# Kernel optimization log

Measured on AMD Instinct MI355X. Metric: run time of the kernel, lower is better.

## Reference

```python
import jax, jax.numpy as jnp
import numpy as np

V, E, U, D = 32000, 128, 256, 256
B, T = 128, 1024


def setup_inputs() -> dict:
    key = jax.random.key(0)
    k_tok, k_emb, k_wk, k_wr, k_wd = jax.random.split(key, 5)
    tokens = jax.random.randint(k_tok, (B, T), 0, V, dtype=jnp.int32)
    emb_table = jax.random.normal(k_emb, (V, E), dtype=jnp.float32) * 0.02
    Wk = jax.random.normal(k_wk, (E, 4 * U), dtype=jnp.float32) * (1.0 / np.sqrt(E))
    Wr = jax.random.normal(k_wr, (U, 4 * U), dtype=jnp.float32) * (1.0 / np.sqrt(U))
    # Keras unit_forget_bias: forget-gate bias initialized to ones (gate order i,f,g,o)
    b = jnp.concatenate([jnp.zeros((U,), jnp.float32), jnp.ones((U,), jnp.float32), jnp.zeros((2 * U,), jnp.float32)])
    Wd = jax.random.normal(k_wd, (U, D), dtype=jnp.float32) * (1.0 / np.sqrt(U))
    bd = jnp.zeros((D,), jnp.float32)
    return {"tokens": tokens, "emb_table": emb_table, "Wk": Wk, "Wr": Wr, "b": b, "Wd": Wd, "bd": bd}


def _masked_lstm(x, mask, Wk, Wr, b):
    # x: [B,T,E], mask: [B,T] bool. Keras semantics: masked steps pass
    # previous h as output and leave (h, c) unchanged.
    units = Wr.shape[0]
    bsz = x.shape[0]
    xT = jnp.swapaxes(x, 0, 1)          # [T,B,E]
    mT = jnp.swapaxes(mask, 0, 1)       # [T,B]

    def step(carry, inp):
        h, c = carry
        xt, mt = inp
        z = xt @ Wk + h @ Wr + b        # [B,4U]
        i, f, g, o = jnp.split(z, 4, axis=-1)
        i = jax.nn.sigmoid(i)
        f = jax.nn.sigmoid(f)
        g = jnp.tanh(g)
        o = jax.nn.sigmoid(o)
        c_new = f * c + i * g
        h_new = o * jnp.tanh(c_new)
        m = mt[:, None]
        h2 = jnp.where(m, h_new, h)
        c2 = jnp.where(m, c_new, c)
        return (h2, c2), h2

    h0 = jnp.zeros((bsz, units), x.dtype)
    c0 = jnp.zeros((bsz, units), x.dtype)
    _, outs = jax.lax.scan(step, (h0, c0), (xT, mT))
    return jnp.swapaxes(outs, 0, 1)     # [B,T,U]


def reference(tokens, emb_table, Wk, Wr, b, Wd, bd):
    # Embedding (mask_zero=True); dropout layers are identity at inference.
    x = emb_table[tokens]               # [B,T,E]
    mask = tokens != 0                  # [B,T]
    h = _masked_lstm(x, mask, Wk, Wr, b)  # [B,T,U]
    y = jax.nn.relu(h @ Wd + bd)        # TimeDistributed Dense(relu) -> [B,T,D]
    return y
```

## Files before the change

### kernel.cpp

```cpp
#include <hip/hip_runtime.h>
#include <cstddef>


typedef unsigned int u32x4 __attribute__((ext_vector_type(4)));

constexpr int TLEN = 1024;
constexpr int EDIM = 128;
constexpr int UDIM = 256;
constexpr int DDIM = 256;

constexpr int BPB  = 8;
constexpr int UPB  = 8;
constexpr int ZCOL = 32;
constexpr int HXROW = 432;
constexpr int ZROW = 36;

__device__ unsigned long long g_pktA[2][128][256];
__device__ unsigned long long g_pktB[2][128][256];

__device__ __forceinline__ int pidx(int k) { return ((k >> 5) * 36) + (k & 31); }

__device__ __forceinline__ u32x4 pkt_load_ic(const unsigned long long* p) {
  u32x4 v;
  asm volatile("global_load_dwordx4 %0, %1, off sc0 sc1" : "=v"(v) : "v"(p));
  return v;
}
__device__ __forceinline__ u32x4 pkt_load_l2(const unsigned long long* p) {
  u32x4 v;
  asm volatile("global_load_dwordx4 %0, %1, off sc0" : "=v"(v) : "v"(p));
  return v;
}
#define PKT_WAIT4(a, b, c, d) \
  asm volatile("s_waitcnt vmcnt(0)" : "+v"(a), "+v"(b), "+v"(c), "+v"(d) :: "memory")
#define TAGS_OK() \
  ((p0[1] == want) & (p0[3] == want) & (p1[1] == want) & (p1[3] == want) & \
   (p2[1] == want) & (p2[3] == want) & (p3[1] == want) & (p3[3] == want))

__device__ __forceinline__ float rowsum16(float v) {
  v += __int_as_float(
      __builtin_amdgcn_mov_dpp(__float_as_int(v), 0x121, 0xf, 0xf, true));
  v += __int_as_float(
      __builtin_amdgcn_mov_dpp(__float_as_int(v), 0x122, 0xf, 0xf, true));
  v += __int_as_float(
      __builtin_amdgcn_mov_dpp(__float_as_int(v), 0x124, 0xf, 0xf, true));
  v += __int_as_float(
      __builtin_amdgcn_mov_dpp(__float_as_int(v), 0x128, 0xf, 0xf, true));
  return v;
}

__global__ __launch_bounds__(256, 2) void we_lstm(
    const int* __restrict__ tokens, const float* __restrict__ emb,
    const float* __restrict__ Wk, const float* __restrict__ Wr,
    const float* __restrict__ bz, float* __restrict__ out)
{
  __shared__ float hx[2][BPB][HXROW];
  __shared__ float zs[BPB][ZROW];
  __shared__ float bias_s[ZCOL];

  const int tid = threadIdx.x;
  const int bid = blockIdx.x;
  const int bg  = ((bid & 7) << 1) | ((bid >> 8) & 1);
  const int ug  = (bid >> 3) & 31;
  const int b0  = bg * BPB;
  const int u0  = ug * UPB;

  const int ksl = tid & 15;
  const int cq  = (tid >> 4) & 7;
  const int bh  = tid >> 7;

  float w[96];
#pragma unroll
  for (int i = 0; i < 6; ++i)
#pragma unroll
    for (int j = 0; j < 4; ++j) {
      const int k = ksl * 4 + i * 64 + j;
#pragma unroll
      for (int cc = 0; cc < 4; ++cc) {
        const int c   = cq * 4 + cc;
        const int col = ((c >> 3) << 8) + u0 + (c & 7);
        w[(i * 4 + j) * 4 + cc] =
            (k < UDIM) ? Wr[k * 1024 + col] : Wk[(k - UDIM) * 1024 + col];
      }
    }
  if (tid < ZCOL) bias_s[tid] = bz[((tid >> 3) << 8) + u0 + (tid & 7)];

  float creg = 0.f;
  const int gb = tid >> 3, gu = tid & 7;
  const int xb = tid >> 5, xe = (tid & 31) << 2;
  const int up = tid & 127, bq = (tid >> 7) * 4;

  bool use_local = true;

  float4 xv = *(const float4*)&emb[(size_t)tokens[(b0 + xb) * TLEN] * EDIM + xe];
  int tk_g = (tid < 64) ? tokens[(b0 + gb) * TLEN] : 1;

  for (int it = 0; it < TLEN; ++it) {
    const int cur = it & 1;

    *(float4*)&hx[cur][xb][pidx(UDIM + xe)] = xv;
    __syncthreads();

    float acc[4][4];
#pragma unroll
    for (int r = 0; r < 4; ++r) {
      acc[r][0] = 0.f; acc[r][1] = 0.f; acc[r][2] = 0.f; acc[r][3] = 0.f;
    }
#pragma unroll
    for (int i = 4; i < 6; ++i) {
      const int hoff = pidx(ksl * 4 + i * 64);
      float4 hv[4];
#pragma unroll
      for (int r = 0; r < 4; ++r)
        hv[r] = *(const float4*)&hx[cur][bh * 4 + r][hoff];
#pragma unroll
      for (int j = 0; j < 4; ++j)
#pragma unroll
        for (int r = 0; r < 4; ++r) {
          const float hval = (j == 0) ? hv[r].x : (j == 1) ? hv[r].y
                             : (j == 2) ? hv[r].z : hv[r].w;
#pragma unroll
          for (int cc = 0; cc < 4; ++cc)
            acc[r][cc] += hval * w[(i * 4 + j) * 4 + cc];
        }
    }

    u32x4 p0, p1, p2, p3;
    const unsigned want = (unsigned)it;
    const int rp = (it + 1) & 1;
    if (it > 0) {
      if (use_local) {
        p0 = pkt_load_l2(&g_pktA[rp][b0 + bq + 0][2 * up]);
        p1 = pkt_load_l2(&g_pktA[rp][b0 + bq + 1][2 * up]);
        p2 = pkt_load_l2(&g_pktA[rp][b0 + bq + 2][2 * up]);
        p3 = pkt_load_l2(&g_pktA[rp][b0 + bq + 3][2 * up]);
      } else {
        p0 = pkt_load_ic(&g_pktB[rp][b0 + bq + 0][2 * up]);
        p1 = pkt_load_ic(&g_pktB[rp][b0 + bq + 1][2 * up]);
        p2 = pkt_load_ic(&g_pktB[rp][b0 + bq + 2][2 * up]);
        p3 = pkt_load_ic(&g_pktB[rp][b0 + bq + 3][2 * up]);
      }
    }

    float4 xv_n;
    int tk_g_n = 1;
    if (it + 1 < TLEN) {
      const int tk_x = tokens[(b0 + xb) * TLEN + it + 1];
      xv_n = *(const float4*)&emb[(size_t)tk_x * EDIM + xe];
      if (tid < 64) tk_g_n = tokens[(b0 + gb) * TLEN + it + 1];
    }

    const int ho = pidx(2 * up);
    if (it > 0) {
      PKT_WAIT4(p0, p1, p2, p3);
      bool ok = TAGS_OK();
      if (use_local) {
        int rounds = 0;
        while (!ok && rounds < 8) {
          __builtin_amdgcn_s_sleep(1);
          p0 = pkt_load_l2(&g_pktA[rp][b0 + bq + 0][2 * up]);
          p1 = pkt_load_l2(&g_pktA[rp][b0 + bq + 1][2 * up]);
          p2 = pkt_load_l2(&g_pktA[rp][b0 + bq + 2][2 * up]);
          p3 = pkt_load_l2(&g_pktA[rp][b0 + bq + 3][2 * up]);
          PKT_WAIT4(p0, p1, p2, p3);
          ok = TAGS_OK();
          ++rounds;
        }
        if (!ok) use_local = false;
      }
      while (!ok) {
        p0 = pkt_load_ic(&g_pktB[rp][b0 + bq + 0][2 * up]);
        p1 = pkt_load_ic(&g_pktB[rp][b0 + bq + 1][2 * up]);
        p2 = pkt_load_ic(&g_pktB[rp][b0 + bq + 2][2 * up]);
        p3 = pkt_load_ic(&g_pktB[rp][b0 + bq + 3][2 * up]);
        PKT_WAIT4(p0, p1, p2, p3);
        ok = TAGS_OK();
        if (!ok) __builtin_amdgcn_s_sleep(1);
      }
      *(float2*)&hx[cur][bq + 0][ho] =
          make_float2(__uint_as_float(p0[0]), __uint_as_float(p0[2]));
      *(float2*)&hx[cur][bq + 1][ho] =
          make_float2(__uint_as_float(p1[0]), __uint_as_float(p1[2]));
      *(float2*)&hx[cur][bq + 2][ho] =
          make_float2(__uint_as_float(p2[0]), __uint_as_float(p2[2]));
      *(float2*)&hx[cur][bq + 3][ho] =
          make_float2(__uint_as_float(p3[0]), __uint_as_float(p3[2]));
    } else {
#pragma unroll
      for (int jj = 0; jj < 4; ++jj)
        *(float2*)&hx[cur][bq + jj][ho] = make_float2(0.f, 0.f);
    }
    __syncthreads();

#pragma unroll
    for (int i = 0; i < 4; ++i) {
      const int hoff = pidx(ksl * 4 + i * 64);
      float4 hv[4];
#pragma unroll
      for (int r = 0; r < 4; ++r)
        hv[r] = *(const float4*)&hx[cur][bh * 4 + r][hoff];
#pragma unroll
      for (int j = 0; j < 4; ++j)
#pragma unroll
        for (int r = 0; r < 4; ++r) {
          const float hval = (j == 0) ? hv[r].x : (j == 1) ? hv[r].y
                             : (j == 2) ? hv[r].z : hv[r].w;
#pragma unroll
          for (int cc = 0; cc < 4; ++cc)
            acc[r][cc] += hval * w[(i * 4 + j) * 4 + cc];
        }
    }

#pragma unroll
    for (int r = 0; r < 4; ++r)
#pragma unroll
      for (int cc = 0; cc < 4; ++cc)
        acc[r][cc] = rowsum16(acc[r][cc]);
    if (ksl == 0) {
#pragma unroll
      for (int r = 0; r < 4; ++r)
        *(float4*)&zs[bh * 4 + r][cq * 4] =
            make_float4(acc[r][0], acc[r][1], acc[r][2], acc[r][3]);
    }
    __syncthreads();

    if (tid < 64) {
      const float zi = zs[gb][gu]      + bias_s[gu];
      const float zf = zs[gb][8 + gu]  + bias_s[8 + gu];
      const float zg = zs[gb][16 + gu] + bias_s[16 + gu];
      const float zo = zs[gb][24 + gu] + bias_s[24 + gu];
      const float gi = 1.f / (1.f + __expf(-zi));
      const float gf = 1.f / (1.f + __expf(-zf));
      const float gg = 1.f - 2.f / (1.f + __expf(2.f * zg));
      const float go = 1.f / (1.f + __expf(-zo));
      const float cn = gf * creg + gi * gg;
      const float th = 1.f - 2.f / (1.f + __expf(2.f * cn));
      const float hn = go * th;
      const bool msk = (tk_g != 0);
      const float hold = hx[cur][gb][pidx(u0 + gu)];
      const float h2 = msk ? hn : hold;
      creg = msk ? cn : creg;
      const unsigned long long pkt =
          ((unsigned long long)(unsigned)(it + 1) << 32) | __float_as_uint(h2);
      __hip_atomic_store(&g_pktA[cur][b0 + gb][u0 + gu], pkt, __ATOMIC_RELAXED,
                         __HIP_MEMORY_SCOPE_WORKGROUP);
      __hip_atomic_store(&g_pktB[cur][b0 + gb][u0 + gu], pkt, __ATOMIC_RELAXED,
                         __HIP_MEMORY_SCOPE_AGENT);
      __builtin_nontemporal_store(
          h2, &out[((size_t)(b0 + gb) * TLEN + it) * DDIM + u0 + gu]);
    }
    xv = xv_n;
    tk_g = tk_g_n;
  }
}

__global__ __launch_bounds__(256, 2) void we_proj(
    const float* __restrict__ Wd, const float* __restrict__ bd,
    float* __restrict__ out)
{
  __shared__ float hs[32][260];
  __shared__ float ws[32][260];
  __shared__ float bds[DDIM];

  const int tid = threadIdx.x;
  const size_t row0 = (size_t)blockIdx.x * 32;

#pragma unroll
  for (int j2 = 0; j2 < 8; ++j2) {
    const int idx = tid + j2 * 256;
    const int r = idx >> 6;
    const int cq = idx & 63;
    *(float4*)&hs[r][cq * 4] = *(const float4*)&out[(row0 + r) * DDIM + cq * 4];
  }
  bds[tid] = bd[tid];

  const int rg = tid >> 5;
  const int c0 = (tid & 31) * 8;
  float acc[4][8];
#pragma unroll
  for (int i = 0; i < 4; ++i)
#pragma unroll
    for (int c = 0; c < 8; ++c) acc[i][c] = 0.f;

  for (int kt = 0; kt < 8; ++kt) {
    __syncthreads();
#pragma unroll
    for (int j2 = 0; j2 < 8; ++j2) {
      const int idx = tid + j2 * 256;
      const int kk = idx >> 6;
      const int cq = idx & 63;
      *(float4*)&ws[kk][cq * 4] =
          *(const float4*)&Wd[(size_t)(kt * 32 + kk) * DDIM + cq * 4];
    }
    __syncthreads();
#pragma unroll
    for (int kk = 0; kk < 32; ++kk) {
      const float4 wv0 = *(const float4*)&ws[kk][c0];
      const float4 wv1 = *(const float4*)&ws[kk][c0 + 4];
#pragma unroll
      for (int i = 0; i < 4; ++i) {
        const float hval = hs[rg + i * 8][kt * 32 + kk];
        acc[i][0] += hval * wv0.x; acc[i][1] += hval * wv0.y;
        acc[i][2] += hval * wv0.z; acc[i][3] += hval * wv0.w;
        acc[i][4] += hval * wv1.x; acc[i][5] += hval * wv1.y;
        acc[i][6] += hval * wv1.z; acc[i][7] += hval * wv1.w;
      }
    }
  }
#pragma unroll
  for (int i = 0; i < 4; ++i) {
    float4 y0, y1;
    y0.x = fmaxf(acc[i][0] + bds[c0 + 0], 0.f);
    y0.y = fmaxf(acc[i][1] + bds[c0 + 1], 0.f);
    y0.z = fmaxf(acc[i][2] + bds[c0 + 2], 0.f);
    y0.w = fmaxf(acc[i][3] + bds[c0 + 3], 0.f);
    y1.x = fmaxf(acc[i][4] + bds[c0 + 4], 0.f);
    y1.y = fmaxf(acc[i][5] + bds[c0 + 5], 0.f);
    y1.z = fmaxf(acc[i][6] + bds[c0 + 6], 0.f);
    y1.w = fmaxf(acc[i][7] + bds[c0 + 7], 0.f);
    const size_t orow = (row0 + rg + i * 8) * DDIM;
    *(float4*)&out[orow + c0]     = y0;
    *(float4*)&out[orow + c0 + 4] = y1;
  }
}

extern "C" void kernel_launch(void* const* d_in, const int* in_sizes, int n_in,
                              void* d_out, int out_size, void* d_ws, size_t ws_size,
                              hipStream_t stream) {
  const int*   tokens = (const int*)d_in[0];
  const float* emb    = (const float*)d_in[1];
  const float* Wk     = (const float*)d_in[2];
  const float* Wr     = (const float*)d_in[3];
  const float* bz     = (const float*)d_in[4];
  const float* Wd     = (const float*)d_in[5];
  const float* bd     = (const float*)d_in[6];
  float* out = (float*)d_out;
  (void)in_sizes; (void)n_in; (void)out_size; (void)d_ws; (void)ws_size;
  hipLaunchKernelGGL(we_lstm, dim3(512), dim3(256), 0, stream,
                     tokens, emb, Wk, Wr, bz, out);
  hipLaunchKernelGGL(we_proj, dim3(128 * TLEN / 32), dim3(256), 0, stream,
                     Wd, bd, out);
}
```

Measured before the change: 3.696 ms.

## Interleave two batch groups per block to hide cross-block h exchange latency

Each workgroup now handles two 8-row batch groups (A and B) in alternation instead of one, halving the grid to 256 blocks with occupancy 1. While one group computes its recurrent matvec, the packet loads for the other group's previous hidden state are already in flight. This hides the inter-block polling latency behind useful compute. The cost is fewer resident waves and the loss of the earlier split where the input-projection part was computed before the wait. The spin-retry budget on the local L2 path is also doubled.

```diff
diff --git a/kernel.cpp b/kernel.cpp
--- a/kernel.cpp
+++ b/kernel.cpp
@@ -48,7 +48,7 @@
   return v;
 }
 
-__global__ __launch_bounds__(256, 2) void we_lstm(
+__global__ __launch_bounds__(256, 1) void we_lstm(
     const int* __restrict__ tokens, const float* __restrict__ emb,
     const float* __restrict__ Wk, const float* __restrict__ Wr,
     const float* __restrict__ bz, float* __restrict__ out)
@@ -59,9 +59,10 @@
 
   const int tid = threadIdx.x;
   const int bid = blockIdx.x;
-  const int bg  = ((bid & 7) << 1) | ((bid >> 8) & 1);
-  const int ug  = (bid >> 3) & 31;
-  const int b0  = bg * BPB;
+  const int pg  = bid & 7;
+  const int ug  = bid >> 3;
+  const int b0A = pg * 16;
+  const int b0B = pg * 16 + 8;
   const int u0  = ug * UPB;
 
   const int ksl = tid & 15;
@@ -84,20 +85,69 @@
     }
   if (tid < ZCOL) bias_s[tid] = bz[((tid >> 3) << 8) + u0 + (tid & 7)];
 
-  float creg = 0.f;
+  float cregA = 0.f, cregB = 0.f;
   const int gb = tid >> 3, gu = tid & 7;
   const int xb = tid >> 5, xe = (tid & 31) << 2;
   const int up = tid & 127, bq = (tid >> 7) * 4;
 
   bool use_local = true;
 
-  float4 xv = *(const float4*)&emb[(size_t)tokens[(b0 + xb) * TLEN] * EDIM + xe];
-  int tk_g = (tid < 64) ? tokens[(b0 + gb) * TLEN] : 1;
-
-  for (int it = 0; it < TLEN; ++it) {
-    const int cur = it & 1;
-
-    *(float4*)&hx[cur][xb][pidx(UDIM + xe)] = xv;
+  float4 xvA = *(const float4*)&emb[(size_t)tokens[(b0A + xb) * TLEN] * EDIM + xe];
+  float4 xvB = *(const float4*)&emb[(size_t)tokens[(b0B + xb) * TLEN] * EDIM + xe];
+  int tkA = (tid < 64) ? tokens[(b0A + gb) * TLEN] : 1;
+  int tkB = (tid < 64) ? tokens[(b0B + gb) * TLEN] : 1;
+
+  u32x4 pA0, pA1, pA2, pA3, pB0, pB1, pB2, pB3;
+
+  auto run_phase = [&](const int b0c, float (*hxc)[HXROW], float& creg,
+                       int& tk_g, float4& xv,
+                       u32x4& p0, u32x4& p1, u32x4& p2, u32x4& p3,
+                       const int b0n,
+                       u32x4& q0, u32x4& q1, u32x4& q2, u32x4& q3,
+                       const int it, const int itn) {
+    const int rp = (it + 1) & 1;
+    const unsigned want = (unsigned)it;
+    const int ho = pidx(2 * up);
+
+    if (it > 0) {
+      PKT_WAIT4(p0, p1, p2, p3);
+      bool ok = TAGS_OK();
+      if (!ok && use_local) {
+        int rounds = 0;
+        do {
+          __builtin_amdgcn_s_sleep(1);
+          p0 = pkt_load_l2(&g_pktA[rp][b0c + bq + 0][2 * up]);
+          p1 = pkt_load_l2(&g_pktA[rp][b0c + bq + 1][2 * up]);
+          p2 = pkt_load_l2(&g_pktA[rp][b0c + bq + 2][2 * up]);
+          p3 = pkt_load_l2(&g_pktA[rp][b0c + bq + 3][2 * up]);
+          PKT_WAIT4(p0, p1, p2, p3);
+          ok = TAGS_OK();
+        } while (!ok && ++rounds < 16);
+        if (!ok) use_local = false;
+      }
+      while (!ok) {
+        p0 = pkt_load_ic(&g_pktB[rp][b0c + bq + 0][2 * up]);
+        p1 = pkt_load_ic(&g_pktB[rp][b0c + bq + 1][2 * up]);
+        p2 = pkt_load_ic(&g_pktB[rp][b0c + bq + 2][2 * up]);
+        p3 = pkt_load_ic(&g_pktB[rp][b0c + bq + 3][2 * up]);
+        PKT_WAIT4(p0, p1, p2, p3);
+        ok = TAGS_OK();
+        if (!ok) __builtin_amdgcn_s_sleep(1);
+      }
+      *(float2*)&hxc[bq + 0][ho] =
+          make_float2(__uint_as_float(p0[0]), __uint_as_float(p0[2]));
+      *(float2*)&hxc[bq + 1][ho] =
+          make_float2(__uint_as_float(p1[0]), __uint_as_float(p1[2]));
+      *(float2*)&hxc[bq + 2][ho] =
+          make_float2(__uint_as_float(p2[0]), __uint_as_float(p2[2]));
+      *(float2*)&hxc[bq + 3][ho] =
+          make_float2(__uint_as_float(p3[0]), __uint_as_float(p3[2]));
+    } else {
+#pragma unroll
+      for (int jj = 0; jj < 4; ++jj)
+        *(float2*)&hxc[bq + jj][ho] = make_float2(0.f, 0.f);
+    }
+    *(float4*)&hxc[xb][pidx(UDIM + xe)] = xv;
     __syncthreads();
 
     float acc[4][4];
@@ -106,12 +156,12 @@
       acc[r][0] = 0.f; acc[r][1] = 0.f; acc[r][2] = 0.f; acc[r][3] = 0.f;
     }
 #pragma unroll
-    for (int i = 4; i < 6; ++i) {
+    for (int i = 0; i < 6; ++i) {
       const int hoff = pidx(ksl * 4 + i * 64);
       float4 hv[4];
 #pragma unroll
       for (int r = 0; r < 4; ++r)
-        hv[r] = *(const float4*)&hx[cur][bh * 4 + r][hoff];
+        hv[r] = *(const float4*)&hxc[bh * 4 + r][hoff];
 #pragma unroll
       for (int j = 0; j < 4; ++j)
 #pragma unroll
@@ -124,90 +174,27 @@
         }
     }
 
-    u32x4 p0, p1, p2, p3;
-    const unsigned want = (unsigned)it;
-    const int rp = (it + 1) & 1;
-    if (it > 0) {
+    if (itn > 0 && itn < TLEN) {
+      const int rpn = (itn + 1) & 1;
       if (use_local) {
-        p0 = pkt_load_l2(&g_pktA[rp][b0 + bq + 0][2 * up]);
-        p1 = pkt_load_l2(&g_pktA[rp][b0 + bq + 1][2 * up]);
-        p2 = pkt_load_l2(&g_pktA[rp][b0 + bq + 2][2 * up]);
-        p3 = pkt_load_l2(&g_pktA[rp][b0 + bq + 3][2 * up]);
+        q0 = pkt_load_l2(&g_pktA[rpn][b0n + bq + 0][2 * up]);
+        q1 = pkt_load_l2(&g_pktA[rpn][b0n + bq + 1][2 * up]);
+        q2 = pkt_load_l2(&g_pktA[rpn][b0n + bq + 2][2 * up]);
+        q3 = pkt_load_l2(&g_pktA[rpn][b0n + bq + 3][2 * up]);
       } else {
-        p0 = pkt_load_ic(&g_pktB[rp][b0 + bq + 0][2 * up]);
-        p1 = pkt_load_ic(&g_pktB[rp][b0 + bq + 1][2 * up]);
-        p2 = pkt_load_ic(&g_pktB[rp][b0 + bq + 2][2 * up]);
-        p3 = pkt_load_ic(&g_pktB[rp][b0 + bq + 3][2 * up]);
+        q0 = pkt_load_ic(&g_pktB[rpn][b0n + bq + 0][2 * up]);
+        q1 = pkt_load_ic(&g_pktB[rpn][b0n + bq + 1][2 * up]);
+        q2 = pkt_load_ic(&g_pktB[rpn][b0n + bq + 2][2 * up]);
+        q3 = pkt_load_ic(&g_pktB[rpn][b0n + bq + 3][2 * up]);
       }
     }
 
     float4 xv_n;
-    int tk_g_n = 1;
+    int tk_n = 1;
     if (it + 1 < TLEN) {
-      const int tk_x = tokens[(b0 + xb) * TLEN + it + 1];
+      const int tk_x = tokens[(b0c + xb) * TLEN + it + 1];
       xv_n = *(const float4*)&emb[(size_t)tk_x * EDIM + xe];
-      if (tid < 64) tk_g_n = tokens[(b0 + gb) * TLEN + it + 1];
-    }
-
-    const int ho = pidx(2 * up);
-    if (it > 0) {
-      PKT_WAIT4(p0, p1, p2, p3);
-      bool ok = TAGS_OK();
-      if (use_local) {
-        int rounds = 0;
-        while (!ok && rounds < 8) {
-          __builtin_amdgcn_s_sleep(1);
-          p0 = pkt_load_l2(&g_pktA[rp][b0 + bq + 0][2 * up]);
-          p1 = pkt_load_l2(&g_pktA[rp][b0 + bq + 1][2 * up]);
-          p2 = pkt_load_l2(&g_pktA[rp][b0 + bq + 2][2 * up]);
-          p3 = pkt_load_l2(&g_pktA[rp][b0 + bq + 3][2 * up]);
-          PKT_WAIT4(p0, p1, p2, p3);
-          ok = TAGS_OK();
-          ++rounds;
-        }
-        if (!ok) use_local = false;
-      }
-      while (!ok) {
-        p0 = pkt_load_ic(&g_pktB[rp][b0 + bq + 0][2 * up]);
-        p1 = pkt_load_ic(&g_pktB[rp][b0 + bq + 1][2 * up]);
-        p2 = pkt_load_ic(&g_pktB[rp][b0 + bq + 2][2 * up]);
-        p3 = pkt_load_ic(&g_pktB[rp][b0 + bq + 3][2 * up]);
-        PKT_WAIT4(p0, p1, p2, p3);
-        ok = TAGS_OK();
-        if (!ok) __builtin_amdgcn_s_sleep(1);
-      }
-      *(float2*)&hx[cur][bq + 0][ho] =
-          make_float2(__uint_as_float(p0[0]), __uint_as_float(p0[2]));
-      *(float2*)&hx[cur][bq + 1][ho] =
-          make_float2(__uint_as_float(p1[0]), __uint_as_float(p1[2]));
-      *(float2*)&hx[cur][bq + 2][ho] =
-          make_float2(__uint_as_float(p2[0]), __uint_as_float(p2[2]));
-      *(float2*)&hx[cur][bq + 3][ho] =
-          make_float2(__uint_as_float(p3[0]), __uint_as_float(p3[2]));
-    } else {
-#pragma unroll
-      for (int jj = 0; jj < 4; ++jj)
-        *(float2*)&hx[cur][bq + jj][ho] = make_float2(0.f, 0.f);
-    }
-    __syncthreads();
-
-#pragma unroll
-    for (int i = 0; i < 4; ++i) {
-      const int hoff = pidx(ksl * 4 + i * 64);
-      float4 hv[4];
-#pragma unroll
-      for (int r = 0; r < 4; ++r)
-        hv[r] = *(const float4*)&hx[cur][bh * 4 + r][hoff];
-#pragma unroll
-      for (int j = 0; j < 4; ++j)
-#pragma unroll
-        for (int r = 0; r < 4; ++r) {
-          const float hval = (j == 0) ? hv[r].x : (j == 1) ? hv[r].y
-                             : (j == 2) ? hv[r].z : hv[r].w;
-#pragma unroll
-          for (int cc = 0; cc < 4; ++cc)
-            acc[r][cc] += hval * w[(i * 4 + j) * 4 + cc];
-        }
+      if (tid < 64) tk_n = tokens[(b0c + gb) * TLEN + it + 1];
     }
 
 #pragma unroll
@@ -236,20 +223,27 @@
       const float th = 1.f - 2.f / (1.f + __expf(2.f * cn));
       const float hn = go * th;
       const bool msk = (tk_g != 0);
-      const float hold = hx[cur][gb][pidx(u0 + gu)];
+      const float hold = hxc[gb][pidx(u0 + gu)];
       const float h2 = msk ? hn : hold;
       creg = msk ? cn : creg;
       const unsigned long long pkt =
           ((unsigned long long)(unsigned)(it + 1) << 32) | __float_as_uint(h2);
-      __hip_atomic_store(&g_pktA[cur][b0 + gb][u0 + gu], pkt, __ATOMIC_RELAXED,
-                         __HIP_MEMORY_SCOPE_WORKGROUP);
-      __hip_atomic_store(&g_pktB[cur][b0 + gb][u0 + gu], pkt, __ATOMIC_RELAXED,
-                         __HIP_MEMORY_SCOPE_AGENT);
+      __hip_atomic_store(&g_pktA[it & 1][b0c + gb][u0 + gu], pkt,
+                         __ATOMIC_RELAXED, __HIP_MEMORY_SCOPE_WORKGROUP);
+      __hip_atomic_store(&g_pktB[it & 1][b0c + gb][u0 + gu], pkt,
+                         __ATOMIC_RELAXED, __HIP_MEMORY_SCOPE_AGENT);
       __builtin_nontemporal_store(
-          h2, &out[((size_t)(b0 + gb) * TLEN + it) * DDIM + u0 + gu]);
+          h2, &out[((size_t)(b0c + gb) * TLEN + it) * DDIM + u0 + gu]);
     }
     xv = xv_n;
-    tk_g = tk_g_n;
+    tk_g = tk_n;
+  };
+
+  for (int it = 0; it < TLEN; ++it) {
+    run_phase(b0A, hx[0], cregA, tkA, xvA, pA0, pA1, pA2, pA3,
+              b0B, pB0, pB1, pB2, pB3, it, it);
+    run_phase(b0B, hx[1], cregB, tkB, xvB, pB0, pB1, pB2, pB3,
+              b0A, pA0, pA1, pA2, pA3, it, it + 1);
   }
 }
 
@@ -335,7 +329,7 @@
   const float* bd     = (const float*)d_in[6];
   float* out = (float*)d_out;
   (void)in_sizes; (void)n_in; (void)out_size; (void)d_ws; (void)ws_size;
-  hipLaunchKernelGGL(we_lstm, dim3(512), dim3(256), 0, stream,
+  hipLaunchKernelGGL(we_lstm, dim3(256), dim3(256), 0, stream,
                      tokens, emb, Wk, Wr, bz, out);
   hipLaunchKernelGGL(we_proj, dim3(128 * TLEN / 32), dim3(256), 0, stream,
                      Wd, bd, out);
```

Result: slower. 5.233 ms (+41.6%).

## Reorder LSTM step loop to issue packet loads early and prestage next x

Applied to the files above, without the earlier changes.

Restructures the per-timestep loop of the persistent LSTM kernel. The packet loads for the next step's h values are now issued right after this step's h is published, rather than after the x-part matmul. The next x embedding is written into the other hx buffer ahead of time, so the x and h products become one 6-chunk loop and one __syncthreads per step goes away. The local spin limit rises from 8 to 24 rounds. The first packet poll now runs almost immediately after the remote stores, so it is more likely to see stale tags and fall into the sleep/retry path. The longer spin limit is meant to make up for that, at the cost of more polling before falling back to the agent-scope buffer.

```diff
diff --git a/kernel.cpp b/kernel.cpp
--- a/kernel.cpp
+++ b/kernel.cpp
@@ -91,71 +91,33 @@
 
   bool use_local = true;
 
-  float4 xv = *(const float4*)&emb[(size_t)tokens[(b0 + xb) * TLEN] * EDIM + xe];
+  {
+    const int t0 = tokens[(b0 + xb) * TLEN];
+    const float4 x0 = *(const float4*)&emb[(size_t)t0 * EDIM + xe];
+    *(float4*)&hx[0][xb][pidx(UDIM + xe)] = x0;
+  }
+  float4 xv_w;
+  {
+    const int t1 = tokens[(b0 + xb) * TLEN + 1];
+    xv_w = *(const float4*)&emb[(size_t)t1 * EDIM + xe];
+  }
+  int tk_x_next = tokens[(b0 + xb) * TLEN + 2];
   int tk_g = (tid < 64) ? tokens[(b0 + gb) * TLEN] : 1;
+
+  u32x4 p0 = {0,0,0,0}, p1 = {0,0,0,0}, p2 = {0,0,0,0}, p3 = {0,0,0,0};
 
   for (int it = 0; it < TLEN; ++it) {
     const int cur = it & 1;
-
-    *(float4*)&hx[cur][xb][pidx(UDIM + xe)] = xv;
-    __syncthreads();
-
-    float acc[4][4];
-#pragma unroll
-    for (int r = 0; r < 4; ++r) {
-      acc[r][0] = 0.f; acc[r][1] = 0.f; acc[r][2] = 0.f; acc[r][3] = 0.f;
-    }
-#pragma unroll
-    for (int i = 4; i < 6; ++i) {
-      const int hoff = pidx(ksl * 4 + i * 64);
-      float4 hv[4];
-#pragma unroll
-      for (int r = 0; r < 4; ++r)
-        hv[r] = *(const float4*)&hx[cur][bh * 4 + r][hoff];
-#pragma unroll
-      for (int j = 0; j < 4; ++j)
-#pragma unroll
-        for (int r = 0; r < 4; ++r) {
-          const float hval = (j == 0) ? hv[r].x : (j == 1) ? hv[r].y
-                             : (j == 2) ? hv[r].z : hv[r].w;
-#pragma unroll
-          for (int cc = 0; cc < 4; ++cc)
-            acc[r][cc] += hval * w[(i * 4 + j) * 4 + cc];
-        }
-    }
-
-    u32x4 p0, p1, p2, p3;
-    const unsigned want = (unsigned)it;
-    const int rp = (it + 1) & 1;
+    const int ho  = pidx(2 * up);
+
     if (it > 0) {
-      if (use_local) {
-        p0 = pkt_load_l2(&g_pktA[rp][b0 + bq + 0][2 * up]);
-        p1 = pkt_load_l2(&g_pktA[rp][b0 + bq + 1][2 * up]);
-        p2 = pkt_load_l2(&g_pktA[rp][b0 + bq + 2][2 * up]);
-        p3 = pkt_load_l2(&g_pktA[rp][b0 + bq + 3][2 * up]);
-      } else {
-        p0 = pkt_load_ic(&g_pktB[rp][b0 + bq + 0][2 * up]);
-        p1 = pkt_load_ic(&g_pktB[rp][b0 + bq + 1][2 * up]);
-        p2 = pkt_load_ic(&g_pktB[rp][b0 + bq + 2][2 * up]);
-        p3 = pkt_load_ic(&g_pktB[rp][b0 + bq + 3][2 * up]);
-      }
-    }
-
-    float4 xv_n;
-    int tk_g_n = 1;
-    if (it + 1 < TLEN) {
-      const int tk_x = tokens[(b0 + xb) * TLEN + it + 1];
-      xv_n = *(const float4*)&emb[(size_t)tk_x * EDIM + xe];
-      if (tid < 64) tk_g_n = tokens[(b0 + gb) * TLEN + it + 1];
-    }
-
-    const int ho = pidx(2 * up);
-    if (it > 0) {
+      const unsigned want = (unsigned)it;
+      const int rp = (it + 1) & 1;
       PKT_WAIT4(p0, p1, p2, p3);
       bool ok = TAGS_OK();
-      if (use_local) {
+      if (!ok && use_local) {
         int rounds = 0;
-        while (!ok && rounds < 8) {
+        do {
           __builtin_amdgcn_s_sleep(1);
           p0 = pkt_load_l2(&g_pktA[rp][b0 + bq + 0][2 * up]);
           p1 = pkt_load_l2(&g_pktA[rp][b0 + bq + 1][2 * up]);
@@ -163,8 +125,7 @@
           p3 = pkt_load_l2(&g_pktA[rp][b0 + bq + 3][2 * up]);
           PKT_WAIT4(p0, p1, p2, p3);
           ok = TAGS_OK();
-          ++rounds;
-        }
+        } while (!ok && ++rounds < 24);
         if (!ok) use_local = false;
       }
       while (!ok) {
@@ -191,8 +152,16 @@
     }
     __syncthreads();
 
-#pragma unroll
-    for (int i = 0; i < 4; ++i) {
+    if (it + 1 < TLEN)
+      *(float4*)&hx[1 - cur][xb][pidx(UDIM + xe)] = xv_w;
+
+    float acc[4][4];
+#pragma unroll
+    for (int r = 0; r < 4; ++r) {
+      acc[r][0] = 0.f; acc[r][1] = 0.f; acc[r][2] = 0.f; acc[r][3] = 0.f;
+    }
+#pragma unroll
+    for (int i = 0; i < 6; ++i) {
       const int hoff = pidx(ksl * 4 + i * 64);
       float4 hv[4];
 #pragma unroll
@@ -222,6 +191,15 @@
             make_float4(acc[r][0], acc[r][1], acc[r][2], acc[r][3]);
     }
     __syncthreads();
+
+    if (it + 2 < TLEN) {
+      xv_w = *(const float4*)&emb[(size_t)tk_x_next * EDIM + xe];
+      const int nidx = (it + 3 < TLEN) ? it + 3 : TLEN - 1;
+      tk_x_next = tokens[(b0 + xb) * TLEN + nidx];
+    }
+    int tk_g_n = 1;
+    if (tid < 64 && it + 1 < TLEN)
+      tk_g_n = tokens[(b0 + gb) * TLEN + it + 1];
 
     if (tid < 64) {
       const float zi = zs[gb][gu]      + bias_s[gu];
@@ -248,8 +226,22 @@
       __builtin_nontemporal_store(
           h2, &out[((size_t)(b0 + gb) * TLEN + it) * DDIM + u0 + gu]);
     }
-    xv = xv_n;
     tk_g = tk_g_n;
+
+    if (it + 1 < TLEN) {
+      const int rpn = cur;
+      if (use_local) {
+        p0 = pkt_load_l2(&g_pktA[rpn][b0 + bq + 0][2 * up]);
+        p1 = pkt_load_l2(&g_pktA[rpn][b0 + bq + 1][2 * up]);
+        p2 = pkt_load_l2(&g_pktA[rpn][b0 + bq + 2][2 * up]);
+        p3 = pkt_load_l2(&g_pktA[rpn][b0 + bq + 3][2 * up]);
+      } else {
+        p0 = pkt_load_ic(&g_pktB[rpn][b0 + bq + 0][2 * up]);
+        p1 = pkt_load_ic(&g_pktB[rpn][b0 + bq + 1][2 * up]);
+        p2 = pkt_load_ic(&g_pktB[rpn][b0 + bq + 2][2 * up]);
+        p3 = pkt_load_ic(&g_pktB[rpn][b0 + bq + 3][2 * up]);
+      }
+    }
   }
 }
 
```

Measured after the change: 7.196 ms. 1.95x slower.
